# Kernel tuning notes

Hardware: AMD Instinct MI355X
Metric: run time of the kernel (lower is better)

## Reference

```python
import jax, jax.numpy as jnp
import numpy as np

SIGMA = 1.0  # kernel bandwidth (init kwarg)

VS = 4096   # src vertices
VT = 4096   # tar vertices
FS = 8192   # src triangles
FT = 8192   # tar triangles
FR = 8192   # reference triangles


def setup_inputs() -> dict:
    key = jax.random.key(0)
    k0, k1, k2, k3, k4, k5 = jax.random.split(key, 6)
    src_vertices = jax.random.normal(k0, (VS, 3), dtype=jnp.float32)
    src_indices = jax.random.randint(k1, (FS, 3), 0, VS, dtype=jnp.int64)
    tar_vertices = jax.random.normal(k2, (VT, 3), dtype=jnp.float32)
    tar_indices = jax.random.randint(k3, (FT, 3), 0, VT, dtype=jnp.int64)
    ref_normals = 0.1 * jax.random.normal(k4, (FR, 3), dtype=jnp.float32)
    ref_centers = jax.random.normal(k5, (FR, 3), dtype=jnp.float32)
    return {
        "src_vertices": src_vertices,
        "src_indices": src_indices,
        "tar_vertices": tar_vertices,
        "tar_indices": tar_indices,
        "ref_normals": ref_normals,
        "ref_centers": ref_centers,
    }


def _tri_normals_centers(vertices, indices):
    tris = vertices[indices]               # [F, 3, 3]
    a, b, c = tris[:, 0, :], tris[:, 1, :], tris[:, 2, :]
    normals = 0.5 * jnp.cross(a - b, c - b)  # [F, 3]
    centers = tris.sum(axis=1) / 3.0         # [F, 3]
    return normals, centers


def _sqdist(src, tar):
    # d[i, j] = ||tar_i - src_j||^2  -> shape [Nt, Ns]
    s2 = jnp.sum(src * src, axis=-1)  # [Ns]
    t2 = jnp.sum(tar * tar, axis=-1)  # [Nt]
    return t2[:, None] + s2[None, :] - 2.0 * (tar @ src.T)


def _cauchy(d):
    return 1.0 / (1.0 + d / SIGMA) ** 2


def _energy(sn, sc, tn, tc):
    e1 = jnp.sum((sn @ sn.T) * _cauchy(_sqdist(sc, sc)))
    e2 = jnp.sum((tn @ sn.T) * _cauchy(_sqdist(sc, tc)))
    e3 = jnp.sum((tn @ tn.T) * _cauchy(_sqdist(tc, tc)))
    return e1 - 2.0 * e2 + e3


def reference(src_vertices, src_indices, tar_vertices, tar_indices, ref_normals, ref_centers):
    src_n, src_c = _tri_normals_centers(src_vertices, src_indices)
    tar_n, tar_c = _tri_normals_centers(tar_vertices, tar_indices)
    energy = _energy(src_n, src_c, ref_normals, ref_centers)
    energy = energy + _energy(tar_n, tar_c, ref_normals, ref_centers)
    energy = energy + 0.8 * _energy(src_n, src_c, tar_n, tar_c)
    return energy
```

## Files before the change

kernel.cpp:

```cpp
#include <hip/hip_runtime.h>

#define NSEG 8192
#define NPTS (3 * NSEG)
#define NSUP 96
#define NY   49

typedef short bf16x8 __attribute__((ext_vector_type(8)));
typedef float f32x16 __attribute__((ext_vector_type(16)));
typedef unsigned short u16;

__device__ __forceinline__ u16 f2bf(float x) {
    unsigned u = __builtin_bit_cast(unsigned, x);
    return (u16)((u + 0x7FFFu + ((u >> 16) & 1u)) >> 16);
}
__device__ __forceinline__ float bf2f(u16 h) {
    unsigned u = ((unsigned)h) << 16;
    return __builtin_bit_cast(float, u);
}

__device__ __forceinline__ void compute_point(
    int seg, int f,
    const float* __restrict__ sv, const int* __restrict__ si,
    const float* __restrict__ tv, const int* __restrict__ ti,
    const float* __restrict__ rn, const float* __restrict__ rc,
    float& cx, float& cy, float& cz, float& nx, float& ny, float& nz)
{
    if (seg == 2) {
        nx = rn[3*f];   ny = rn[3*f+1]; nz = rn[3*f+2];
        cx = rc[3*f];   cy = rc[3*f+1]; cz = rc[3*f+2];
    } else {
        const float* v  = (seg == 0) ? sv : tv;
        const int*   nd = (seg == 0) ? si : ti;
        int i0 = nd[3*f], i1 = nd[3*f+1], i2 = nd[3*f+2];
        float ax = v[3*i0], ay = v[3*i0+1], az = v[3*i0+2];
        float bx = v[3*i1], by = v[3*i1+1], bz = v[3*i1+2];
        float gx = v[3*i2], gy = v[3*i2+1], gz = v[3*i2+2];
        float ux = ax-bx, uy = ay-by, uz = az-bz;
        float wx = gx-bx, wy = gy-by, wz = gz-bz;
        nx = 0.5f*(uy*wz - uz*wy);
        ny = 0.5f*(uz*wx - ux*wz);
        nz = 0.5f*(ux*wy - uy*wx);
        cx = (ax+bx+gx)*(1.0f/3.0f);
        cy = (ay+by+gy)*(1.0f/3.0f);
        cz = (az+bz+gz)*(1.0f/3.0f);
    }
}

__global__ void setup_feats(const float* __restrict__ sv, const int* __restrict__ si,
                            const float* __restrict__ tv, const int* __restrict__ ti,
                            const float* __restrict__ rn, const float* __restrict__ rc,
                            u16* __restrict__ ws, float* __restrict__ out) {
    int p = blockIdx.x * 256 + threadIdx.x;
    if (p == 0) out[0] = 0.0f;
    if (p >= NPTS) return;
    int seg = p >> 13, f = p & (NSEG - 1);
    float cx, cy, cz, nx, ny, nz;
    compute_point(seg, f, sv, si, tv, ti, rn, rc, cx, cy, cz, nx, ny, nz);

    const u16 ONE = 0x3F80;
    float s = cx*cx + cy*cy + cz*cz;
    u16 chx = f2bf(cx), chy = f2bf(cy), chz = f2bf(cz);
    u16 clx = f2bf(cx - bf2f(chx)), cly = f2bf(cy - bf2f(chy)), clz = f2bf(cz - bf2f(chz));
    u16 sh  = f2bf(s);
    u16 sl  = f2bf(s - bf2f(sh));
    u16 m2hx = f2bf(-2.0f*bf2f(chx)), m2hy = f2bf(-2.0f*bf2f(chy)), m2hz = f2bf(-2.0f*bf2f(chz));
    u16 m2lx = f2bf(-2.0f*bf2f(clx)), m2ly = f2bf(-2.0f*bf2f(cly)), m2lz = f2bf(-2.0f*bf2f(clz));
    u16 nhx = f2bf(nx), nhy = f2bf(ny), nhz = f2bf(nz);
    u16 nlx = f2bf(nx - bf2f(nhx)), nly = f2bf(ny - bf2f(nhy)), nlz = f2bf(nz - bf2f(nhz));

    u16 at[16] = {chx,chy,chz, clx,cly,clz, chx,chy,chz, sh, sl, ONE, ONE, ONE, 0, 0};
    u16 bt[16] = {m2hx,m2hy,m2hz, m2hx,m2hy,m2hz, m2lx,m2ly,m2lz, ONE, ONE, sh, sl, ONE, 0, 0};
    u16 an[16] = {nhx,nhy,nhz, nlx,nly,nlz, nhx,nhy,nhz, 0,0,0,0,0,0,0};
    u16 bn[16] = {nhx,nhy,nhz, nhx,nhy,nhz, nlx,nly,nlz, 0,0,0,0,0,0,0};

    bf16x8* A8 = (bf16x8*)ws;
    bf16x8* B8 = A8 + (size_t)NPTS*4;
    bf16x8 v0, v1, v2, v3;
    #pragma unroll
    for (int k = 0; k < 8; ++k) { v0[k] = (short)at[k]; v1[k] = (short)at[k+8];
                                  v2[k] = (short)an[k]; v3[k] = (short)an[k+8]; }
    A8[(size_t)p*4+0] = v0; A8[(size_t)p*4+1] = v1; A8[(size_t)p*4+2] = v2; A8[(size_t)p*4+3] = v3;
    #pragma unroll
    for (int k = 0; k < 8; ++k) { v0[k] = (short)bt[k]; v1[k] = (short)bt[k+8];
                                  v2[k] = (short)bn[k]; v3[k] = (short)bn[k+8]; }
    B8[(size_t)p*4+0] = v0; B8[(size_t)p*4+1] = v1; B8[(size_t)p*4+2] = v2; B8[(size_t)p*4+3] = v3;
}

__launch_bounds__(512, 3)
__global__ void energy_mfma(const u16* __restrict__ ws, float* __restrict__ out) {
    const int tid  = threadIdx.x;
    const int lane = tid & 63, wid = tid >> 6;
    const int half = lane >> 5, r32 = lane & 31;

    const int X = blockIdx.x;
    const int Y = blockIdx.y;
    int J = X + Y; if (J >= NSUP) J -= NSUP;
    const int gi = X >> 5;
    const int gj = J >> 5;

    const float Wt[9] = {1.8f, -0.8f, -1.0f,
                        -0.8f,  1.8f, -1.0f,
                        -1.0f, -1.0f,  2.0f};
    const float mult = (Y == 0 || Y == 48) ? 1.0f : 2.0f;
    const float w = Wt[gi*3 + gj] * mult;

    const bf16x8* A8 = (const bf16x8*)ws;
    const bf16x8* B8 = A8 + (size_t)NPTS*4;

    const int pi = X*256 + wid*32 + r32;
    const bf16x8 at = A8[pi*4 + half];
    const bf16x8 an = A8[pi*4 + 2 + half];

    f32x16 Z;
    #pragma unroll
    for (int k = 0; k < 16; ++k) Z[k] = 0.0f;

    const int base = J*1024 + r32*4 + half;

    bf16x8 btf = B8[base];
    bf16x8 bnf = B8[base + 2];

    float ts0 = 0.0f, ts1 = 0.0f;
    #pragma unroll 2
    for (int jt = 0; jt < 8; ++jt) {
        int nofs = base + ((jt < 7) ? (jt + 1) : jt) * 128;
        bf16x8 nbt = B8[nofs];
        bf16x8 nbn = B8[nofs + 2];

        f32x16 ct = __builtin_amdgcn_mfma_f32_32x32x16_bf16(at, btf, Z, 0, 0, 0);
        f32x16 cn = __builtin_amdgcn_mfma_f32_32x32x16_bf16(an, bnf, Z, 0, 0, 0);

        #pragma unroll
        for (int g = 0; g < 4; ++g) {
            float t0 = ct[4*g+0], t1 = ct[4*g+1], t2 = ct[4*g+2], t3 = ct[4*g+3];
            float q0 = t0*t0, q1 = t1*t1, q2 = t2*t2, q3 = t3*t3;
            float s01 = q0*q1, s23 = q2*q3;
            float r   = __builtin_amdgcn_rcpf(s01*s23);
            float u   = __builtin_fmaf(cn[4*g+1], q0, cn[4*g+0]*q1);
            float v   = __builtin_fmaf(cn[4*g+3], q2, cn[4*g+2]*q3);
            float num = __builtin_fmaf(v, s01, u*s23);
            if (g & 1) ts1 = __builtin_fmaf(num, r, ts1);
            else       ts0 = __builtin_fmaf(num, r, ts0);
        }

        btf = nbt; bnf = nbn;
    }
    float acc = w * (ts0 + ts1);

    for (int off = 32; off; off >>= 1) acc += __shfl_down(acc, off, 64);
    __shared__ float partial[8];
    if ((tid & 63) == 0) partial[wid] = acc;
    __syncthreads();
    if (tid == 0) {
        float s = ((partial[0] + partial[1]) + (partial[2] + partial[3]))
                + ((partial[4] + partial[5]) + (partial[6] + partial[7]));
        atomicAdd(out, s);
    }
}

extern "C" void kernel_launch(void* const* d_in, const int* in_sizes, int n_in,
                              void* d_out, int out_size, void* d_ws, size_t ws_size,
                              hipStream_t stream) {
    const float* sv = (const float*)d_in[0];
    const int*   si = (const int*)d_in[1];
    const float* tv = (const float*)d_in[2];
    const int*   ti = (const int*)d_in[3];
    const float* rn = (const float*)d_in[4];
    const float* rc = (const float*)d_in[5];
    float* out = (float*)d_out;
    u16*   ws  = (u16*)d_ws;

    setup_feats<<<NPTS/256, 256, 0, stream>>>(sv, si, tv, ti, rn, rc, ws, out);
    dim3 grid(NSUP, NY);
    energy_mfma<<<grid, 512, 0, stream>>>(ws, out);
}
```

Baseline: 133.8 us.

## Regroup energy blocks: 256-thread blocks each covering four diagonal offsets

Each block now handles half a 256-row super-tile (128 rows) and loops over four consecutive diagonal offsets, instead of one 512-thread block per (row super-tile, offset) pair. The grid drops from 96x49 blocks to 192x13, which cuts the number of atomics and block launches and keeps the A fragments in registers across four column tiles. The trade-off is longer serial work per block, fewer and smaller blocks (2496 blocks of 4 waves), and an unbalanced tail because the last y-group does only one offset.

```diff
diff --git a/kernel.cpp b/kernel.cpp
--- a/kernel.cpp
+++ b/kernel.cpp
@@ -3,7 +3,8 @@
 #define NSEG 8192
 #define NPTS (3 * NSEG)
 #define NSUP 96
-#define NY   49
+#define NXB  192
+#define NYG  13
 
 typedef short bf16x8 __attribute__((ext_vector_type(8)));
 typedef float f32x16 __attribute__((ext_vector_type(16)));
@@ -86,28 +87,27 @@
     B8[(size_t)p*4+0] = v0; B8[(size_t)p*4+1] = v1; B8[(size_t)p*4+2] = v2; B8[(size_t)p*4+3] = v3;
 }
 
-__launch_bounds__(512, 3)
+__launch_bounds__(256, 3)
 __global__ void energy_mfma(const u16* __restrict__ ws, float* __restrict__ out) {
     const int tid  = threadIdx.x;
     const int lane = tid & 63, wid = tid >> 6;
     const int half = lane >> 5, r32 = lane & 31;
 
-    const int X = blockIdx.x;
-    const int Y = blockIdx.y;
-    int J = X + Y; if (J >= NSUP) J -= NSUP;
+    const int bx = blockIdx.x;
+    const int X  = bx >> 1;
+    const int g  = blockIdx.y;
+    const int y0  = (g < 12) ? 4*g : 48;
+    const int ycnt = (g < 12) ? 4 : 1;
     const int gi = X >> 5;
-    const int gj = J >> 5;
 
     const float Wt[9] = {1.8f, -0.8f, -1.0f,
                         -0.8f,  1.8f, -1.0f,
                         -1.0f, -1.0f,  2.0f};
-    const float mult = (Y == 0 || Y == 48) ? 1.0f : 2.0f;
-    const float w = Wt[gi*3 + gj] * mult;
 
     const bf16x8* A8 = (const bf16x8*)ws;
     const bf16x8* B8 = A8 + (size_t)NPTS*4;
 
-    const int pi = X*256 + wid*32 + r32;
+    const int pi = X*256 + (bx & 1)*128 + wid*32 + r32;
     const bf16x8 at = A8[pi*4 + half];
     const bf16x8 an = A8[pi*4 + 2 + half];
 
@@ -115,47 +115,54 @@
     #pragma unroll
     for (int k = 0; k < 16; ++k) Z[k] = 0.0f;
 
-    const int base = J*1024 + r32*4 + half;
+    const int lofs = r32*4 + half;
 
-    bf16x8 btf = B8[base];
-    bf16x8 bnf = B8[base + 2];
+    float acc = 0.0f;
+    for (int yy = 0; yy < ycnt; ++yy) {
+        const int y = y0 + yy;
+        int J = X + y; if (J >= NSUP) J -= NSUP;
+        const float mult = (y == 0 || y == 48) ? 1.0f : 2.0f;
+        const float w = Wt[gi*3 + (J >> 5)] * mult;
 
-    float ts0 = 0.0f, ts1 = 0.0f;
-    #pragma unroll 2
-    for (int jt = 0; jt < 8; ++jt) {
-        int nofs = base + ((jt < 7) ? (jt + 1) : jt) * 128;
-        bf16x8 nbt = B8[nofs];
-        bf16x8 nbn = B8[nofs + 2];
+        const int base = J*1024 + lofs;
 
-        f32x16 ct = __builtin_amdgcn_mfma_f32_32x32x16_bf16(at, btf, Z, 0, 0, 0);
-        f32x16 cn = __builtin_amdgcn_mfma_f32_32x32x16_bf16(an, bnf, Z, 0, 0, 0);
+        bf16x8 btf = B8[base];
+        bf16x8 bnf = B8[base + 2];
 
-        #pragma unroll
-        for (int g = 0; g < 4; ++g) {
-            float t0 = ct[4*g+0], t1 = ct[4*g+1], t2 = ct[4*g+2], t3 = ct[4*g+3];
-            float q0 = t0*t0, q1 = t1*t1, q2 = t2*t2, q3 = t3*t3;
-            float s01 = q0*q1, s23 = q2*q3;
-            float r   = __builtin_amdgcn_rcpf(s01*s23);
-            float u   = __builtin_fmaf(cn[4*g+1], q0, cn[4*g+0]*q1);
-            float v   = __builtin_fmaf(cn[4*g+3], q2, cn[4*g+2]*q3);
-            float num = __builtin_fmaf(v, s01, u*s23);
-            if (g & 1) ts1 = __builtin_fmaf(num, r, ts1);
-            else       ts0 = __builtin_fmaf(num, r, ts0);
+        float ts0 = 0.0f, ts1 = 0.0f;
+        #pragma unroll 2
+        for (int jt = 0; jt < 8; ++jt) {
+            int nofs = base + ((jt < 7) ? (jt + 1) : jt) * 128;
+            bf16x8 nbt = B8[nofs];
+            bf16x8 nbn = B8[nofs + 2];
+
+            f32x16 ct = __builtin_amdgcn_mfma_f32_32x32x16_bf16(at, btf, Z, 0, 0, 0);
+            f32x16 cn = __builtin_amdgcn_mfma_f32_32x32x16_bf16(an, bnf, Z, 0, 0, 0);
+
+            #pragma unroll
+            for (int gq = 0; gq < 4; ++gq) {
+                float t0 = ct[4*gq+0], t1 = ct[4*gq+1], t2 = ct[4*gq+2], t3 = ct[4*gq+3];
+                float q0 = t0*t0, q1 = t1*t1, q2 = t2*t2, q3 = t3*t3;
+                float s01 = q0*q1, s23 = q2*q3;
+                float r   = __builtin_amdgcn_rcpf(s01*s23);
+                float u   = __builtin_fmaf(cn[4*gq+1], q0, cn[4*gq+0]*q1);
+                float v   = __builtin_fmaf(cn[4*gq+3], q2, cn[4*gq+2]*q3);
+                float num = __builtin_fmaf(v, s01, u*s23);
+                if (gq & 1) ts1 = __builtin_fmaf(num, r, ts1);
+                else        ts0 = __builtin_fmaf(num, r, ts0);
+            }
+
+            btf = nbt; bnf = nbn;
         }
-
-        btf = nbt; bnf = nbn;
+        acc = __builtin_fmaf(w, ts0 + ts1, acc);
     }
-    float acc = w * (ts0 + ts1);
 
     for (int off = 32; off; off >>= 1) acc += __shfl_down(acc, off, 64);
-    __shared__ float partial[8];
+    __shared__ float partial[4];
     if ((tid & 63) == 0) partial[wid] = acc;
     __syncthreads();
-    if (tid == 0) {
-        float s = ((partial[0] + partial[1]) + (partial[2] + partial[3]))
-                + ((partial[4] + partial[5]) + (partial[6] + partial[7]));
-        atomicAdd(out, s);
-    }
+    if (tid == 0)
+        atomicAdd(out, (partial[0] + partial[1]) + (partial[2] + partial[3]));
 }
 
 extern "C" void kernel_launch(void* const* d_in, const int* in_sizes, int n_in,
@@ -171,6 +178,6 @@
     u16*   ws  = (u16*)d_ws;
 
     setup_feats<<<NPTS/256, 256, 0, stream>>>(sv, si, tv, ti, rn, rc, ws, out);
-    dim3 grid(NSUP, NY);
-    energy_mfma<<<grid, 512, 0, stream>>>(ws, out);
+    dim3 grid(NXB, NYG);
+    energy_mfma<<<grid, 256, 0, stream>>>(ws, out);
 }
```

New measurement: 118.6 us. 11.4% less time.
